# Performance work log

Hardware: AMD Instinct MI355X
Metric: run time of the kernel (lower is better)

The kernel has to match this reference:

```python
import jax, jax.numpy as jnp
import numpy as np

B, T, E = 1024, 200, 128
H = 64

def setup_inputs() -> dict:
    key = jax.random.key(0)
    k1, k2, k3, k4 = jax.random.split(key, 4)
    return {
        "query": jax.random.normal(k1, (B, 1, E), dtype=jnp.float32),
        "keys": jax.random.normal(k2, (B, T, E), dtype=jnp.float32),
        "W0": jax.random.normal(k3, (4 * E, H), dtype=jnp.float32) * 0.05,
        "b0": jnp.zeros((H,), dtype=jnp.float32),
        "W1": jax.random.normal(k4, (H, 1), dtype=jnp.float32) * 0.05,
        "b1": jnp.zeros((1,), dtype=jnp.float32),
    }

def reference(query, keys, W0, b0, W1, b1):
    # query: [B,1,E] broadcast to [B,T,E] (repeat_elements along axis 1)
    q = jnp.broadcast_to(query, keys.shape)
    # dnn_input: [B,T,4E] = concat([q, k, q-k, q*k])
    x = jnp.concatenate([q, keys, q - keys, q * keys], axis=-1)
    # one hidden layer with relu, then linear scorer -> [B,T,1]
    h = jax.nn.relu(jnp.einsum('btd,dh->bth', x, W0) + b0)
    att_score = jnp.einsum('bth,ho->bto', h, W1) + b1
    return att_score
```

## Files before the change

kernel.cpp:

```cpp
#include <hip/hip_runtime.h>
#include <hip/hip_bf16.h>


#define TB 200
#define EB 128
#define HB 64

typedef __attribute__((ext_vector_type(8))) short bf16x8;
typedef __attribute__((ext_vector_type(4))) float f32x4;

__global__ __launch_bounds__(256, 4)
void lau_kernel(const float* __restrict__ query,
                const float* __restrict__ keys,
                const float* __restrict__ W0,
                const float* __restrict__ b0,
                const float* __restrict__ W1,
                const float* __restrict__ b1,
                float* __restrict__ out)
{
    const int b   = blockIdx.x;
    const int tid = threadIdx.x;

    __shared__ float q_s[EB];
    __shared__ float bias_s[HB];
    __shared__ float w1_s[HB];
    __shared__ float red_s[256];
    __shared__ __align__(16) __hip_bfloat16 wbt[HB][EB + 8];

    if (tid < EB) q_s[tid] = query[(size_t)b * EB + tid];
    __syncthreads();

    {
        const int h     = tid & 63;
        const int chunk = tid >> 6;
        float biasp = 0.f;
        #pragma unroll 8
        for (int i = 0; i < 32; ++i) {
            const int e = chunk * 32 + i;
            const float qe  = q_s[e];
            const float w0a = W0[(size_t)e            * HB + h];
            const float w0b = W0[(size_t)(EB + e)     * HB + h];
            const float w0c = W0[(size_t)(2 * EB + e) * HB + h];
            const float w0d = W0[(size_t)(3 * EB + e) * HB + h];
            wbt[h][e] = __float2bfloat16(w0b - w0c + qe * w0d);
            biasp += qe * (w0a + w0c);
        }
        red_s[tid] = biasp;
    }
    __syncthreads();
    if (tid < HB) {
        bias_s[tid] = red_s[tid] + red_s[tid + 64] + red_s[tid + 128] + red_s[tid + 192] + b0[tid];
        w1_s[tid]   = W1[tid];
    }
    __syncthreads();

    const int lane = tid & 63;
    const int wave = tid >> 6;
    const int ln15 = lane & 15;
    const int quad = lane >> 4;

    float w1q[4], biasq[4];
    #pragma unroll
    for (int nt = 0; nt < 4; ++nt) {
        w1q[nt]   = w1_s[nt * 16 + ln15];
        biasq[nt] = bias_s[nt * 16 + ln15];
    }

    const __hip_bfloat16* wb_base = &wbt[ln15][quad * 8];

    const float* kb  = keys + (size_t)b * TB * EB;
    const float  b1v = b1[0];

    for (int mt = wave; mt < 13; mt += 4) {
        const int mrow = mt * 16 + ln15;
        const int mc   = mrow < TB ? mrow : TB - 1;
        const float* arow = kb + (size_t)mc * EB + quad * 8;

        f32x4 acc[4] = {{0,0,0,0},{0,0,0,0},{0,0,0,0},{0,0,0,0}};
        #pragma unroll
        for (int ks = 0; ks < 4; ++ks) {
            const float4 a0 = *(const float4*)(arow + ks * 32);
            const float4 a1 = *(const float4*)(arow + ks * 32 + 4);
            union { bf16x8 v; __hip_bfloat162 h2[4]; } u;
            u.h2[0] = __float22bfloat162_rn(make_float2(a0.x, a0.y));
            u.h2[1] = __float22bfloat162_rn(make_float2(a0.z, a0.w));
            u.h2[2] = __float22bfloat162_rn(make_float2(a1.x, a1.y));
            u.h2[3] = __float22bfloat162_rn(make_float2(a1.z, a1.w));
            #pragma unroll
            for (int nt = 0; nt < 4; ++nt) {
                const bf16x8 bf = *(const bf16x8*)(wb_base + nt * 16 * (EB + 8) + ks * 32);
                acc[nt] = __builtin_amdgcn_mfma_f32_16x16x32_bf16(u.v, bf, acc[nt], 0, 0, 0);
            }
        }

        float part[4];
        #pragma unroll
        for (int r = 0; r < 4; ++r) {
            float s = 0.f;
            #pragma unroll
            for (int nt = 0; nt < 4; ++nt) {
                float hv = acc[nt][r] + biasq[nt];
                hv = hv > 0.f ? hv : 0.f;
                s += hv * w1q[nt];
            }
            part[r] = s;
        }
        #pragma unroll
        for (int m = 1; m < 16; m <<= 1) {
            #pragma unroll
            for (int r = 0; r < 4; ++r)
                part[r] += __shfl_xor(part[r], m, 64);
        }
        if (ln15 == 0) {
            #pragma unroll
            for (int r = 0; r < 4; ++r) {
                const int mg = mt * 16 + quad * 4 + r;
                if (mg < TB) out[(size_t)b * TB + mg] = part[r] + b1v;
            }
        }
    }
}

extern "C" void kernel_launch(void* const* d_in, const int* in_sizes, int n_in,
                              void* d_out, int out_size, void* d_ws, size_t ws_size,
                              hipStream_t stream) {
    const float* query = (const float*)d_in[0];
    const float* keys  = (const float*)d_in[1];
    const float* W0    = (const float*)d_in[2];
    const float* b0    = (const float*)d_in[3];
    const float* W1    = (const float*)d_in[4];
    const float* b1    = (const float*)d_in[5];
    float* out = (float*)d_out;

    lau_kernel<<<1024, 256, 0, stream>>>(query, keys, W0, b0, W1, b1, out);
}
```

Measured before the change: 170.4 us.

## Prefetch key tiles ahead of weight folding and software-pipeline the tile loop

Each wave now loads its first key tile before the per-block weight-folding prologue and, inside the loop, issues loads for the next tile before running the MFMAs on the current one. The goal is to hide global-memory latency behind the prologue and the compute. The W0 folding also switches to float4 loads with a 16-way bias reduction through a padded shared array. Launch bounds drop from 4 to 3 blocks per SU, which allows more registers for the prefetch buffers but may lower occupancy. On the last iteration the prefetch redundantly reloads tile 12.

```diff
diff --git a/kernel.cpp b/kernel.cpp
--- a/kernel.cpp
+++ b/kernel.cpp
@@ -9,7 +9,7 @@
 typedef __attribute__((ext_vector_type(8))) short bf16x8;
 typedef __attribute__((ext_vector_type(4))) float f32x4;
 
-__global__ __launch_bounds__(256, 4)
+__global__ __launch_bounds__(256, 3)
 void lau_kernel(const float* __restrict__ query,
                 const float* __restrict__ keys,
                 const float* __restrict__ W0,
@@ -18,46 +18,72 @@
                 const float* __restrict__ b1,
                 float* __restrict__ out)
 {
-    const int b   = blockIdx.x;
-    const int tid = threadIdx.x;
+    const int b    = blockIdx.x;
+    const int tid  = threadIdx.x;
+    const int lane = tid & 63;
+    const int wave = tid >> 6;
+    const int ln15 = lane & 15;
+    const int quad = lane >> 4;
 
     __shared__ float q_s[EB];
     __shared__ float bias_s[HB];
     __shared__ float w1_s[HB];
-    __shared__ float red_s[256];
+    __shared__ float red2[HB][17];
     __shared__ __align__(16) __hip_bfloat16 wbt[HB][EB + 8];
 
+    const float* kb = keys + (size_t)b * TB * EB;
+
     if (tid < EB) q_s[tid] = query[(size_t)b * EB + tid];
+
+    int mt = wave;
+    float4 a[8];
+    {
+        const int mrow = mt * 16 + ln15;
+        const int mc   = mrow < TB ? mrow : TB - 1;
+        const float* arow = kb + (size_t)mc * EB + quad * 8;
+        #pragma unroll
+        for (int ks = 0; ks < 4; ++ks) {
+            a[2*ks]   = *(const float4*)(arow + ks * 32);
+            a[2*ks+1] = *(const float4*)(arow + ks * 32 + 4);
+        }
+    }
     __syncthreads();
 
     {
-        const int h     = tid & 63;
-        const int chunk = tid >> 6;
-        float biasp = 0.f;
-        #pragma unroll 8
-        for (int i = 0; i < 32; ++i) {
-            const int e = chunk * 32 + i;
-            const float qe  = q_s[e];
-            const float w0a = W0[(size_t)e            * HB + h];
-            const float w0b = W0[(size_t)(EB + e)     * HB + h];
-            const float w0c = W0[(size_t)(2 * EB + e) * HB + h];
-            const float w0d = W0[(size_t)(3 * EB + e) * HB + h];
-            wbt[h][e] = __float2bfloat16(w0b - w0c + qe * w0d);
-            biasp += qe * (w0a + w0c);
+        const int hq = (tid & 15) * 4;
+        const int ck = tid >> 4;
+        float bp0 = 0.f, bp1 = 0.f, bp2 = 0.f, bp3 = 0.f;
+        #pragma unroll
+        for (int i = 0; i < 8; ++i) {
+            const int e = ck * 8 + i;
+            const float qe = q_s[e];
+            const float4 wa = *(const float4*)&W0[(size_t)e            * HB + hq];
+            const float4 wb = *(const float4*)&W0[(size_t)(EB + e)     * HB + hq];
+            const float4 wc = *(const float4*)&W0[(size_t)(2 * EB + e) * HB + hq];
+            const float4 wd = *(const float4*)&W0[(size_t)(3 * EB + e) * HB + hq];
+            wbt[hq + 0][e] = __float2bfloat16(wb.x - wc.x + qe * wd.x);
+            wbt[hq + 1][e] = __float2bfloat16(wb.y - wc.y + qe * wd.y);
+            wbt[hq + 2][e] = __float2bfloat16(wb.z - wc.z + qe * wd.z);
+            wbt[hq + 3][e] = __float2bfloat16(wb.w - wc.w + qe * wd.w);
+            bp0 += qe * (wa.x + wc.x);
+            bp1 += qe * (wa.y + wc.y);
+            bp2 += qe * (wa.z + wc.z);
+            bp3 += qe * (wa.w + wc.w);
         }
-        red_s[tid] = biasp;
+        red2[hq + 0][ck] = bp0;
+        red2[hq + 1][ck] = bp1;
+        red2[hq + 2][ck] = bp2;
+        red2[hq + 3][ck] = bp3;
     }
     __syncthreads();
     if (tid < HB) {
-        bias_s[tid] = red_s[tid] + red_s[tid + 64] + red_s[tid + 128] + red_s[tid + 192] + b0[tid];
+        float s = b0[tid];
+        #pragma unroll
+        for (int c = 0; c < 16; ++c) s += red2[tid][c];
+        bias_s[tid] = s;
         w1_s[tid]   = W1[tid];
     }
     __syncthreads();
-
-    const int lane = tid & 63;
-    const int wave = tid >> 6;
-    const int ln15 = lane & 15;
-    const int quad = lane >> 4;
 
     float w1q[4], biasq[4];
     #pragma unroll
@@ -67,25 +93,28 @@
     }
 
     const __hip_bfloat16* wb_base = &wbt[ln15][quad * 8];
+    const float b1v = b1[0];
 
-    const float* kb  = keys + (size_t)b * TB * EB;
-    const float  b1v = b1[0];
-
-    for (int mt = wave; mt < 13; mt += 4) {
-        const int mrow = mt * 16 + ln15;
-        const int mc   = mrow < TB ? mrow : TB - 1;
-        const float* arow = kb + (size_t)mc * EB + quad * 8;
+    for (; mt < 13; mt += 4) {
+        const int mtn   = (mt + 4 < 13) ? (mt + 4) : 12;
+        const int mrowN = mtn * 16 + ln15;
+        const int mcN   = mrowN < TB ? mrowN : TB - 1;
+        const float* arowN = kb + (size_t)mcN * EB + quad * 8;
+        float4 an[8];
+        #pragma unroll
+        for (int ks = 0; ks < 4; ++ks) {
+            an[2*ks]   = *(const float4*)(arowN + ks * 32);
+            an[2*ks+1] = *(const float4*)(arowN + ks * 32 + 4);
+        }
 
         f32x4 acc[4] = {{0,0,0,0},{0,0,0,0},{0,0,0,0},{0,0,0,0}};
         #pragma unroll
         for (int ks = 0; ks < 4; ++ks) {
-            const float4 a0 = *(const float4*)(arow + ks * 32);
-            const float4 a1 = *(const float4*)(arow + ks * 32 + 4);
             union { bf16x8 v; __hip_bfloat162 h2[4]; } u;
-            u.h2[0] = __float22bfloat162_rn(make_float2(a0.x, a0.y));
-            u.h2[1] = __float22bfloat162_rn(make_float2(a0.z, a0.w));
-            u.h2[2] = __float22bfloat162_rn(make_float2(a1.x, a1.y));
-            u.h2[3] = __float22bfloat162_rn(make_float2(a1.z, a1.w));
+            u.h2[0] = __float22bfloat162_rn(make_float2(a[2*ks].x,   a[2*ks].y));
+            u.h2[1] = __float22bfloat162_rn(make_float2(a[2*ks].z,   a[2*ks].w));
+            u.h2[2] = __float22bfloat162_rn(make_float2(a[2*ks+1].x, a[2*ks+1].y));
+            u.h2[3] = __float22bfloat162_rn(make_float2(a[2*ks+1].z, a[2*ks+1].w));
             #pragma unroll
             for (int nt = 0; nt < 4; ++nt) {
                 const bf16x8 bf = *(const bf16x8*)(wb_base + nt * 16 * (EB + 8) + ks * 32);
@@ -118,6 +147,9 @@
                 if (mg < TB) out[(size_t)b * TB + mg] = part[r] + b1v;
             }
         }
+
+        #pragma unroll
+        for (int i = 0; i < 8; ++i) a[i] = an[i];
     }
 }
 
```

New measurement: 176.0 us. 1.03x slower.

## Stage keys tile through LDS as bf16 with coalesced loads and 512 threads

Applied to the files above, without the earlier changes.

Doubles the block to 512 threads (8 waves) and splits the weight-folding prologue across more threads. Each block's whole keys tile is loaded with fully coalesced float4 reads in two halves, converted to bf16, and stored in an LDS buffer that aliases the weight-staging area. Weight fragments are preloaded into registers before that buffer is overwritten. MFMA A-operands are then read from LDS instead of strided global rows. This costs more LDS, extra barriers and more register pressure, and with 13 row tiles over 8 waves some waves get two tiles and others only one.

```diff
diff --git a/kernel.cpp b/kernel.cpp
--- a/kernel.cpp
+++ b/kernel.cpp
@@ -5,11 +5,13 @@
 #define TB 200
 #define EB 128
 #define HB 64
+#define KROW 136
+#define KROWS 208
 
 typedef __attribute__((ext_vector_type(8))) short bf16x8;
 typedef __attribute__((ext_vector_type(4))) float f32x4;
 
-__global__ __launch_bounds__(256, 4)
+__global__ __launch_bounds__(512, 4)
 void lau_kernel(const float* __restrict__ query,
                 const float* __restrict__ keys,
                 const float* __restrict__ W0,
@@ -18,14 +20,23 @@
                 const float* __restrict__ b1,
                 float* __restrict__ out)
 {
-    const int b   = blockIdx.x;
-    const int tid = threadIdx.x;
+    const int b    = blockIdx.x;
+    const int tid  = threadIdx.x;
+    const int lane = tid & 63;
+    const int wave = tid >> 6;
+    const int ln15 = lane & 15;
+    const int quad = lane >> 4;
 
-    __shared__ float q_s[EB];
     __shared__ float bias_s[HB];
     __shared__ float w1_s[HB];
-    __shared__ float red_s[256];
-    __shared__ __align__(16) __hip_bfloat16 wbt[HB][EB + 8];
+    __shared__ __align__(16) unsigned char smem[KROWS * KROW * 2];
+
+    float* q_s   = (float*)smem;
+    float* red_s = (float*)(smem + 512);
+    __hip_bfloat16 (*wbt)[KROW] = (__hip_bfloat16(*)[KROW])(smem + 2560);
+    __hip_bfloat16 (*kt)[KROW]  = (__hip_bfloat16(*)[KROW])smem;
+
+    const float* kb = keys + (size_t)b * TB * EB;
 
     if (tid < EB) q_s[tid] = query[(size_t)b * EB + tid];
     __syncthreads();
@@ -35,8 +46,8 @@
         const int chunk = tid >> 6;
         float biasp = 0.f;
         #pragma unroll 8
-        for (int i = 0; i < 32; ++i) {
-            const int e = chunk * 32 + i;
+        for (int i = 0; i < 16; ++i) {
+            const int e = chunk * 16 + i;
             const float qe  = q_s[e];
             const float w0a = W0[(size_t)e            * HB + h];
             const float w0b = W0[(size_t)(EB + e)     * HB + h];
@@ -49,16 +60,27 @@
     }
     __syncthreads();
     if (tid < HB) {
-        bias_s[tid] = red_s[tid] + red_s[tid + 64] + red_s[tid + 128] + red_s[tid + 192] + b0[tid];
+        float s = b0[tid];
+        #pragma unroll
+        for (int j = 0; j < 8; ++j) s += red_s[tid + 64 * j];
+        bias_s[tid] = s;
         w1_s[tid]   = W1[tid];
     }
     __syncthreads();
 
-    const int lane = tid & 63;
-    const int wave = tid >> 6;
-    const int ln15 = lane & 15;
-    const int quad = lane >> 4;
+    float4 g[7];
+    #pragma unroll
+    for (int j = 0; j < 7; ++j) {
+        const int u = tid + j * 512;
+        if (u < 3200) g[j] = *(const float4*)(kb + (size_t)u * 4);
+    }
 
+    bf16x8 wbf[4][4];
+    #pragma unroll
+    for (int nt = 0; nt < 4; ++nt)
+        #pragma unroll
+        for (int ks = 0; ks < 4; ++ks)
+            wbf[nt][ks] = *(const bf16x8*)&wbt[nt * 16 + ln15][quad * 8 + ks * 32];
     float w1q[4], biasq[4];
     #pragma unroll
     for (int nt = 0; nt < 4; ++nt) {
@@ -66,32 +88,52 @@
         biasq[nt] = bias_s[nt * 16 + ln15];
     }
 
-    const __hip_bfloat16* wb_base = &wbt[ln15][quad * 8];
+    __syncthreads();
 
-    const float* kb  = keys + (size_t)b * TB * EB;
-    const float  b1v = b1[0];
+    #pragma unroll
+    for (int j = 0; j < 7; ++j) {
+        const int u = tid + j * 512;
+        if (u < 3200) {
+            const int row  = u >> 5;
+            const int col4 = (u & 31) * 4;
+            union { uint2 w; __hip_bfloat162 h2[2]; } pk;
+            pk.h2[0] = __float22bfloat162_rn(make_float2(g[j].x, g[j].y));
+            pk.h2[1] = __float22bfloat162_rn(make_float2(g[j].z, g[j].w));
+            *(uint2*)&kt[row][col4] = pk.w;
+        }
+    }
+    #pragma unroll
+    for (int j = 0; j < 7; ++j) {
+        const int u = 3200 + tid + j * 512;
+        if (u < 6400) g[j] = *(const float4*)(kb + (size_t)u * 4);
+    }
+    #pragma unroll
+    for (int j = 0; j < 7; ++j) {
+        const int u = 3200 + tid + j * 512;
+        if (u < 6400) {
+            const int row  = u >> 5;
+            const int col4 = (u & 31) * 4;
+            union { uint2 w; __hip_bfloat162 h2[2]; } pk;
+            pk.h2[0] = __float22bfloat162_rn(make_float2(g[j].x, g[j].y));
+            pk.h2[1] = __float22bfloat162_rn(make_float2(g[j].z, g[j].w));
+            *(uint2*)&kt[row][col4] = pk.w;
+        }
+    }
+    __syncthreads();
 
-    for (int mt = wave; mt < 13; mt += 4) {
-        const int mrow = mt * 16 + ln15;
-        const int mc   = mrow < TB ? mrow : TB - 1;
-        const float* arow = kb + (size_t)mc * EB + quad * 8;
+    const float b1v = b1[0];
+    for (int mt = wave; mt < 13; mt += 8) {
+        bf16x8 af[4];
+        #pragma unroll
+        for (int ks = 0; ks < 4; ++ks)
+            af[ks] = *(const bf16x8*)&kt[mt * 16 + ln15][quad * 8 + ks * 32];
 
         f32x4 acc[4] = {{0,0,0,0},{0,0,0,0},{0,0,0,0},{0,0,0,0}};
         #pragma unroll
-        for (int ks = 0; ks < 4; ++ks) {
-            const float4 a0 = *(const float4*)(arow + ks * 32);
-            const float4 a1 = *(const float4*)(arow + ks * 32 + 4);
-            union { bf16x8 v; __hip_bfloat162 h2[4]; } u;
-            u.h2[0] = __float22bfloat162_rn(make_float2(a0.x, a0.y));
-            u.h2[1] = __float22bfloat162_rn(make_float2(a0.z, a0.w));
-            u.h2[2] = __float22bfloat162_rn(make_float2(a1.x, a1.y));
-            u.h2[3] = __float22bfloat162_rn(make_float2(a1.z, a1.w));
+        for (int ks = 0; ks < 4; ++ks)
             #pragma unroll
-            for (int nt = 0; nt < 4; ++nt) {
-                const bf16x8 bf = *(const bf16x8*)(wb_base + nt * 16 * (EB + 8) + ks * 32);
-                acc[nt] = __builtin_amdgcn_mfma_f32_16x16x32_bf16(u.v, bf, acc[nt], 0, 0, 0);
-            }
-        }
+            for (int nt = 0; nt < 4; ++nt)
+                acc[nt] = __builtin_amdgcn_mfma_f32_16x16x32_bf16(af[ks], wbf[nt][ks], acc[nt], 0, 0, 0);
 
         float part[4];
         #pragma unroll
@@ -132,5 +174,5 @@
     const float* b1    = (const float*)d_in[5];
     float* out = (float*)d_out;
 
-    lau_kernel<<<1024, 256, 0, stream>>>(query, keys, W0, b0, W1, b1, out);
+    lau_kernel<<<1024, 512, 0, stream>>>(query, keys, W0, b0, W1, b1, out);
 }
```

After: 167.6 us. About the same (-1.6%).
